# Kernel optimization log

Measured on AMD Instinct MI355X. Metric: run time of the kernel, lower is better.

The kernel has to match this reference:

```python
import jax, jax.numpy as jnp
import numpy as np

C = 256      # MSA_channels
PC = 256     # pair_channels
G = 4        # groups
GP = C // G  # group_planes
FF = 4 * C
EPS = 1e-5


def layernorm(x, w, b):
    mu = jnp.mean(x, axis=-1, keepdims=True)
    var = jnp.mean(jnp.square(x - mu), axis=-1, keepdims=True)
    return (x - mu) * jax.lax.rsqrt(var + EPS) * w + b


def setup_inputs() -> dict:
    key = jax.random.key(0)
    ks = jax.random.split(key, 12)
    N, D, L = 1, 64, 512
    s = lambda fan_in: 1.0 / np.sqrt(fan_in)
    return {
        "msa_matrix": jax.random.normal(ks[0], (N, D, L, C), jnp.float32),
        "rr_edge": jax.random.normal(ks[1], (N, L, L, PC), jnp.float32),
        "ln_msa_w": jnp.ones((C,), jnp.float32),
        "ln_msa_b": jnp.zeros((C,), jnp.float32),
        "ln_rr_w": jnp.ones((PC,), jnp.float32),
        "ln_rr_b": jnp.zeros((PC,), jnp.float32),
        "WA": jax.random.normal(ks[2], (PC, G), jnp.float32) * s(PC),
        "bA": jnp.zeros((G,), jnp.float32),
        "WV": jax.random.normal(ks[3], (C, C), jnp.float32) * s(C),
        "bV": jnp.zeros((C,), jnp.float32),
        "WO": jax.random.normal(ks[4], (C, C), jnp.float32) * s(C),
        "bO": jnp.zeros((C,), jnp.float32),
        "ln_ff_w": jnp.ones((C,), jnp.float32),
        "ln_ff_b": jnp.zeros((C,), jnp.float32),
        "W1": jax.random.normal(ks[5], (C, FF), jnp.float32) * s(C),
        "b1": jnp.zeros((FF,), jnp.float32),
        "W2": jax.random.normal(ks[6], (FF, C), jnp.float32) * s(FF),
        "b2": jnp.zeros((C,), jnp.float32),
    }


def reference(msa_matrix, rr_edge, ln_msa_w, ln_msa_b, ln_rr_w, ln_rr_b,
              WA, bA, WV, bV, WO, bO, ln_ff_w, ln_ff_b, W1, b1, W2, b2):
    N, D, L, _ = msa_matrix.shape
    raw = msa_matrix
    m = layernorm(msa_matrix, ln_msa_w, ln_msa_b)          # [N,D,L,C]
    E = 0.5 * (rr_edge + jnp.swapaxes(rr_edge, 1, 2))      # symmetrize [N,L,L,PC]
    E = layernorm(E, ln_rr_w, ln_rr_b)
    A = jax.nn.softmax(E @ WA + bA, axis=2)                # [N,L,L,G], softmax over key dim j
    V = (m @ WV + bV).reshape(N, D, L, G, GP)              # [N,D,L,G,GP]
    agg = jnp.einsum('nijg,ndjgc->ndigc', A, V).reshape(N, D, L, C)
    out = agg @ WO + bO
    x = raw + out                                          # residual (dropout = identity at eval)
    h = layernorm(x, ln_ff_w, ln_ff_b)                     # FFN with pre-LN + residual
    return x + (jax.nn.relu(h @ W1 + b1) @ W2 + b2)
```

## Files before the change

### kernel.cpp

```cpp
#include <hip/hip_runtime.h>
#include <hip/hip_bf16.h>

typedef __bf16 bf16;
typedef bf16 bf16x8 __attribute__((ext_vector_type(8)));
typedef bf16 bf16x4v __attribute__((ext_vector_type(4)));
typedef float f32x4 __attribute__((ext_vector_type(4)));

#define LN_EPS 1e-5f

__device__ __forceinline__ void gload_lds16(const bf16* gsrc, bf16* ldst) {
  __builtin_amdgcn_global_load_lds(
      (const __attribute__((address_space(1))) void*)gsrc,
      (__attribute__((address_space(3))) void*)ldst, 16, 0, 0);
}

__global__ __launch_bounds__(256) void ln_rows_kernel(
    const float* __restrict__ in, const float* __restrict__ w,
    const float* __restrict__ b, bf16* __restrict__ out)
{
  int row = blockIdx.x * 4 + (threadIdx.x >> 6);
  int lane = threadIdx.x & 63;
  const float4* p = (const float4*)(in + (size_t)row * 256);
  float4 v = p[lane];
  float s = v.x + v.y + v.z + v.w;
  float q = v.x*v.x + v.y*v.y + v.z*v.z + v.w*v.w;
  #pragma unroll
  for (int o = 32; o; o >>= 1) { s += __shfl_xor(s, o); q += __shfl_xor(q, o); }
  float mu = s * (1.0f/256.0f);
  float rs = rsqrtf(q*(1.0f/256.0f) - mu*mu + LN_EPS);
  float4 wv = ((const float4*)w)[lane];
  float4 bv = ((const float4*)b)[lane];
  bf16x4v o4;
  o4[0] = (bf16)((v.x - mu)*rs*wv.x + bv.x);
  o4[1] = (bf16)((v.y - mu)*rs*wv.y + bv.y);
  o4[2] = (bf16)((v.z - mu)*rs*wv.z + bv.z);
  o4[3] = (bf16)((v.w - mu)*rs*wv.w + bv.w);
  *(bf16x4v*)(out + (size_t)row * 256 + lane * 4) = o4;
}

__global__ __launch_bounds__(256) void transpose_all_kernel(
    const float* __restrict__ WV, const float* __restrict__ WO,
    const float* __restrict__ W1, const float* __restrict__ W2,
    bf16* __restrict__ WVt, bf16* __restrict__ WOt,
    bf16* __restrict__ W1t, bf16* __restrict__ W2t)
{
  __shared__ float tile[32][33];
  int id = blockIdx.x;
  const float* in; bf16* out; int R, C, tpr;
  if (id < 64)       { in = WV; out = WVt; R = 256;  C = 256;  tpr = 8;  }
  else if (id < 128) { in = WO; out = WOt; R = 256;  C = 256;  tpr = 8;  id -= 64; }
  else if (id < 384) { in = W1; out = W1t; R = 256;  C = 1024; tpr = 32; id -= 128; }
  else               { in = W2; out = W2t; R = 1024; C = 256;  tpr = 8;  id -= 384; }
  int bc = (id % tpr) * 32, br = (id / tpr) * 32;
  int tx = threadIdx.x, ty = threadIdx.y;
  #pragma unroll
  for (int i = ty; i < 32; i += 8)
    tile[i][tx] = in[(size_t)(br + i) * C + bc + tx];
  __syncthreads();
  #pragma unroll
  for (int i = ty; i < 32; i += 8)
    out[(size_t)(bc + i) * R + br + tx] = (bf16)tile[tx][i];
}

__global__ __launch_bounds__(256) void sym_ln_wa_kernel(
    const float* __restrict__ rr, const float* __restrict__ w,
    const float* __restrict__ b, const float* __restrict__ WA,
    float* __restrict__ S)
{
  int rem = blockIdx.x; int ti = 0; int len = 32;
  while (rem >= len) { rem -= len; ti++; len--; }
  int tj = ti + rem;
  int wid = threadIdx.x >> 6, lane = threadIdx.x & 63;
  int c0 = lane * 4;
  float4 wv = ((const float4*)w)[lane];
  float4 bv = ((const float4*)b)[lane];
  const float4* wa4 = (const float4*)WA;
  float4 wa0 = wa4[c0+0], wa1 = wa4[c0+1], wa2 = wa4[c0+2], wa3 = wa4[c0+3];
  int pend = blockIdx.y * 64 + 64;
  for (int p = blockIdx.y * 64 + wid; p < pend; p += 4) {
    int i = ti*16 + (p >> 4), j = tj*16 + (p & 15);
    float4 a = ((const float4*)(rr + ((size_t)i*512 + j)*256))[lane];
    float4 c = ((const float4*)(rr + ((size_t)j*512 + i)*256))[lane];
    float ex = 0.5f*(a.x + c.x), ey = 0.5f*(a.y + c.y),
          ez = 0.5f*(a.z + c.z), ew = 0.5f*(a.w + c.w);
    float s = ex+ey+ez+ew;
    float q = ex*ex+ey*ey+ez*ez+ew*ew;
    #pragma unroll
    for (int o = 32; o; o >>= 1) { s += __shfl_xor(s, o); q += __shfl_xor(q, o); }
    float mu = s*(1.f/256.f);
    float rs = rsqrtf(q*(1.f/256.f) - mu*mu + LN_EPS);
    float nx = (ex-mu)*rs*wv.x + bv.x;
    float ny = (ey-mu)*rs*wv.y + bv.y;
    float nz = (ez-mu)*rs*wv.z + bv.z;
    float nw = (ew-mu)*rs*wv.w + bv.w;
    float g0 = nx*wa0.x + ny*wa1.x + nz*wa2.x + nw*wa3.x;
    float g1 = nx*wa0.y + ny*wa1.y + nz*wa2.y + nw*wa3.y;
    float g2 = nx*wa0.z + ny*wa1.z + nz*wa2.z + nw*wa3.z;
    float g3 = nx*wa0.w + ny*wa1.w + nz*wa2.w + nw*wa3.w;
    #pragma unroll
    for (int o = 32; o; o >>= 1) {
      g0 += __shfl_xor(g0, o); g1 += __shfl_xor(g1, o);
      g2 += __shfl_xor(g2, o); g3 += __shfl_xor(g3, o);
    }
    if (lane == 0) {
      float4 r4 = make_float4(g0, g1, g2, g3);
      ((float4*)S)[(size_t)i*512 + j] = r4;
      ((float4*)S)[(size_t)j*512 + i] = r4;
    }
  }
}

__global__ __launch_bounds__(256) void softmax_kernel(
    const float* __restrict__ S, bf16* __restrict__ Aout)
{
  int i = blockIdx.x * 4 + (threadIdx.x >> 6);
  int lane = threadIdx.x & 63;
  const float4* Sr = (const float4*)S + (size_t)i * 512;
  float4 s[8];
  float m0 = -1e30f, m1 = -1e30f, m2 = -1e30f, m3 = -1e30f;
  #pragma unroll
  for (int it = 0; it < 8; it++) {
    s[it] = Sr[lane + it*64];
    m0 = fmaxf(m0, s[it].x); m1 = fmaxf(m1, s[it].y);
    m2 = fmaxf(m2, s[it].z); m3 = fmaxf(m3, s[it].w);
  }
  #pragma unroll
  for (int o = 32; o; o >>= 1) {
    m0 = fmaxf(m0, __shfl_xor(m0, o)); m1 = fmaxf(m1, __shfl_xor(m1, o));
    m2 = fmaxf(m2, __shfl_xor(m2, o)); m3 = fmaxf(m3, __shfl_xor(m3, o));
  }
  float t0=0.f, t1=0.f, t2=0.f, t3=0.f;
  #pragma unroll
  for (int it = 0; it < 8; it++) {
    s[it].x = __expf(s[it].x - m0); t0 += s[it].x;
    s[it].y = __expf(s[it].y - m1); t1 += s[it].y;
    s[it].z = __expf(s[it].z - m2); t2 += s[it].z;
    s[it].w = __expf(s[it].w - m3); t3 += s[it].w;
  }
  #pragma unroll
  for (int o = 32; o; o >>= 1) {
    t0 += __shfl_xor(t0, o); t1 += __shfl_xor(t1, o);
    t2 += __shfl_xor(t2, o); t3 += __shfl_xor(t3, o);
  }
  t0 = 1.f/t0; t1 = 1.f/t1; t2 = 1.f/t2; t3 = 1.f/t3;
  bf16* A0 = Aout + (size_t)i * 512;
  #pragma unroll
  for (int it = 0; it < 8; it++) {
    int j = lane + it*64;
    A0[j]          = (bf16)(s[it].x * t0);
    A0[262144 + j] = (bf16)(s[it].y * t1);
    A0[524288 + j] = (bf16)(s[it].z * t2);
    A0[786432 + j] = (bf16)(s[it].w * t3);
  }
}

template<int MODE>
__global__ __launch_bounds__(256) void gemm_bt_kernel(
    const bf16* __restrict__ Aglob, const bf16* __restrict__ Bglob,
    void* __restrict__ outP, const float* __restrict__ bias,
    const float* __restrict__ resid, int M, int N, int K)
{
  __shared__ bf16 As[128 * 32];
  __shared__ bf16 Bs[128 * 32];
  int g = blockIdx.z;
  const bf16* Ag = Aglob;
  const bf16* Bg = Bglob;
  if (MODE == 1) { Ag += (size_t)g * 512 * 512; Bg += (size_t)g * 4096 * 512; }
  int bm = blockIdx.y * 128, bn = blockIdx.x * 128;
  int tid = threadIdx.x;
  int wid = tid >> 6, lane = tid & 63;
  int wm = (wid >> 1) * 64, wn = (wid & 1) * 64;
  f32x4 acc[4][4];
  #pragma unroll
  for (int mi = 0; mi < 4; mi++)
    #pragma unroll
    for (int ni = 0; ni < 4; ni++)
      acc[mi][ni] = (f32x4){0.f, 0.f, 0.f, 0.f};
  int c0 = wid * 2, c1 = wid * 2 + 1;
  int srow = lane >> 2;
  int scol = (lane & 3) * 8;
  const bf16* a0 = &Ag[(size_t)(bm + c0*16 + srow) * K + scol];
  const bf16* a1 = &Ag[(size_t)(bm + c1*16 + srow) * K + scol];
  const bf16* b0 = &Bg[(size_t)(bn + c0*16 + srow) * K + scol];
  const bf16* b1 = &Bg[(size_t)(bn + c1*16 + srow) * K + scol];
  int fr = lane & 15, fk = (lane >> 4) * 8;
  for (int k0 = 0; k0 < K; k0 += 32) {
    __syncthreads();
    gload_lds16(a0 + k0, &As[c0 * 512]);
    gload_lds16(a1 + k0, &As[c1 * 512]);
    gload_lds16(b0 + k0, &Bs[c0 * 512]);
    gload_lds16(b1 + k0, &Bs[c1 * 512]);
    __syncthreads();
    bf16x8 af[4], bf_[4];
    #pragma unroll
    for (int mi = 0; mi < 4; mi++) af[mi] = *(const bf16x8*)&As[(wm + mi*16 + fr) * 32 + fk];
    #pragma unroll
    for (int ni = 0; ni < 4; ni++) bf_[ni] = *(const bf16x8*)&Bs[(wn + ni*16 + fr) * 32 + fk];
    #pragma unroll
    for (int mi = 0; mi < 4; mi++)
      #pragma unroll
      for (int ni = 0; ni < 4; ni++)
        acc[mi][ni] = __builtin_amdgcn_mfma_f32_16x16x32_bf16(af[mi], bf_[ni], acc[mi][ni], 0, 0, 0);
  }
  int cn0 = lane & 15;
  int rq = (lane >> 4) * 4;
  #pragma unroll
  for (int mi = 0; mi < 4; mi++) {
    #pragma unroll
    for (int ni = 0; ni < 4; ni++) {
      int mb = bm + wm + mi*16 + rq;
      int nc = bn + wn + ni*16 + cn0;
      #pragma unroll
      for (int r = 0; r < 4; r++) {
        int mr = mb + r;
        float v = acc[mi][ni][r];
        if (MODE == 0) {
          v += bias[mr];
          int gg = mr >> 6, rp = mr & 63, d = nc >> 9, j = nc & 511;
          ((bf16*)outP)[((size_t)gg*4096 + d*64 + rp)*512 + j] = (bf16)v;
        } else if (MODE == 1) {
          int d = nc >> 6, c6 = nc & 63;
          ((bf16*)outP)[((size_t)d*512 + mr)*256 + g*64 + c6] = (bf16)v;
        } else {
          v += bias[nc] + resid[(size_t)mr * N + nc];
          ((float*)outP)[(size_t)mr * N + nc] = v;
        }
      }
    }
  }
}

__global__ __launch_bounds__(512, 2) void ffn_fused_kernel(
    const float* __restrict__ x, const float* __restrict__ lnw,
    const float* __restrict__ lnb, const bf16* __restrict__ W1t,
    const float* __restrict__ b1, const bf16* __restrict__ W2t,
    const float* __restrict__ b2, float* __restrict__ out)
{
  __shared__ __align__(16) char hbuf[128 * 512];
  __shared__ __align__(16) char tbuf[128 * 512];
  __shared__ __align__(16) bf16 Bs[256 * 32];
  int tid = threadIdx.x;
  int wid = tid >> 6, lane = tid & 63;
  size_t row0 = (size_t)blockIdx.x * 128;

  {
    float4 wv = ((const float4*)lnw)[lane];
    float4 bv = ((const float4*)lnb)[lane];
    for (int it = 0; it < 16; it++) {
      int row = wid * 16 + it;
      float4 v = ((const float4*)(x + (row0 + row) * 256))[lane];
      float s = v.x+v.y+v.z+v.w, q = v.x*v.x+v.y*v.y+v.z*v.z+v.w*v.w;
      #pragma unroll
      for (int o = 32; o; o >>= 1) { s += __shfl_xor(s, o); q += __shfl_xor(q, o); }
      float mu = s * (1.f/256.f);
      float rs = rsqrtf(q*(1.f/256.f) - mu*mu + LN_EPS);
      bf16x4v o4;
      o4[0] = (bf16)((v.x-mu)*rs*wv.x + bv.x);
      o4[1] = (bf16)((v.y-mu)*rs*wv.y + bv.y);
      o4[2] = (bf16)((v.z-mu)*rs*wv.z + bv.z);
      o4[3] = (bf16)((v.w-mu)*rs*wv.w + bv.w);
      *(bf16x4v*)(hbuf + row*512 + ((lane*8) ^ ((row & 7) << 4))) = o4;
    }
  }
  __syncthreads();

  int wm = (wid >> 2) * 64;
  int wn = (wid & 3) * 64;
  int fr = lane & 15;
  int fk2 = ((lane >> 4) * 8) * 2;
  int cn0 = lane & 15, rq = (lane >> 4) * 4;
  int arow[4], asw[4], boff[4];
  #pragma unroll
  for (int mi = 0; mi < 4; mi++) {
    arow[mi] = wm + mi*16 + fr;
    asw[mi]  = (arow[mi] & 7) << 4;
  }
  #pragma unroll
  for (int ni = 0; ni < 4; ni++) {
    int br = wn + ni*16 + fr;
    boff[ni] = br*64 + (fk2 ^ (((br >> 1) & 3) << 4));
  }
  int srow = tid >> 2;
  int ps = tid & 3;

  f32x4 acc2[4][4];
  #pragma unroll
  for (int mi = 0; mi < 4; mi++)
    #pragma unroll
    for (int ni = 0; ni < 4; ni++)
      acc2[mi][ni] = (f32x4){0.f, 0.f, 0.f, 0.f};

  for (int cf = 0; cf < 4; cf++) {
    f32x4 acc1[4][4];
    #pragma unroll
    for (int mi = 0; mi < 4; mi++)
      #pragma unroll
      for (int ni = 0; ni < 4; ni++)
        acc1[mi][ni] = (f32x4){0.f, 0.f, 0.f, 0.f};
    for (int k0 = 0; k0 < 256; k0 += 32) {
      __syncthreads();
      #pragma unroll
      for (int q = 0; q < 2; q++) {
        int r = q*128 + srow;
        int ls = ps ^ ((r >> 1) & 3);
        gload_lds16(W1t + (size_t)(cf*256 + r) * 256 + k0 + ls*8,
                    Bs + q*4096 + wid*512);
      }
      __syncthreads();
      bf16x8 af[4], bf_[4];
      #pragma unroll
      for (int mi = 0; mi < 4; mi++)
        af[mi] = *(const bf16x8*)(hbuf + arow[mi]*512 + ((k0*2 + fk2) ^ asw[mi]));
      #pragma unroll
      for (int ni = 0; ni < 4; ni++)
        bf_[ni] = *(const bf16x8*)((const char*)Bs + boff[ni]);
      #pragma unroll
      for (int mi = 0; mi < 4; mi++)
        #pragma unroll
        for (int ni = 0; ni < 4; ni++)
          acc1[mi][ni] = __builtin_amdgcn_mfma_f32_16x16x32_bf16(af[mi], bf_[ni], acc1[mi][ni], 0, 0, 0);
    }
    __syncthreads();
    #pragma unroll
    for (int ni = 0; ni < 4; ni++) {
      int col = wn + ni*16 + cn0;
      float bb = b1[cf*256 + col];
      #pragma unroll
      for (int mi = 0; mi < 4; mi++) {
        #pragma unroll
        for (int r = 0; r < 4; r++) {
          int row = wm + mi*16 + rq + r;
          float v = fmaxf(acc1[mi][ni][r] + bb, 0.f);
          *(bf16*)(tbuf + row*512 + ((col*2) ^ ((row & 7) << 4))) = (bf16)v;
        }
      }
    }
    for (int k0 = 0; k0 < 256; k0 += 32) {
      __syncthreads();
      #pragma unroll
      for (int q = 0; q < 2; q++) {
        int r = q*128 + srow;
        int ls = ps ^ ((r >> 1) & 3);
        gload_lds16(W2t + (size_t)r * 1024 + cf*256 + k0 + ls*8,
                    Bs + q*4096 + wid*512);
      }
      __syncthreads();
      bf16x8 af[4], bf_[4];
      #pragma unroll
      for (int mi = 0; mi < 4; mi++)
        af[mi] = *(const bf16x8*)(tbuf + arow[mi]*512 + ((k0*2 + fk2) ^ asw[mi]));
      #pragma unroll
      for (int ni = 0; ni < 4; ni++)
        bf_[ni] = *(const bf16x8*)((const char*)Bs + boff[ni]);
      #pragma unroll
      for (int mi = 0; mi < 4; mi++)
        #pragma unroll
        for (int ni = 0; ni < 4; ni++)
          acc2[mi][ni] = __builtin_amdgcn_mfma_f32_16x16x32_bf16(af[mi], bf_[ni], acc2[mi][ni], 0, 0, 0);
    }
  }
  #pragma unroll
  for (int ni = 0; ni < 4; ni++) {
    int col = wn + ni*16 + cn0;
    float bb = b2[col];
    #pragma unroll
    for (int mi = 0; mi < 4; mi++) {
      #pragma unroll
      for (int r = 0; r < 4; r++) {
        size_t grow = row0 + wm + mi*16 + rq + r;
        out[grow*256 + col] = x[grow*256 + col] + acc2[mi][ni][r] + bb;
      }
    }
  }
}

extern "C" void kernel_launch(void* const* d_in, const int* in_sizes, int n_in,
                              void* d_out, int out_size, void* d_ws, size_t ws_size,
                              hipStream_t stream)
{
  (void)in_sizes; (void)n_in; (void)out_size; (void)ws_size;
  const float* msa = (const float*)d_in[0];
  const float* rr  = (const float*)d_in[1];
  const float* lmw = (const float*)d_in[2];
  const float* lmb = (const float*)d_in[3];
  const float* lrw = (const float*)d_in[4];
  const float* lrb = (const float*)d_in[5];
  const float* WA  = (const float*)d_in[6];
  const float* WV  = (const float*)d_in[8];
  const float* bV  = (const float*)d_in[9];
  const float* WO  = (const float*)d_in[10];
  const float* bO  = (const float*)d_in[11];
  const float* lfw = (const float*)d_in[12];
  const float* lfb = (const float*)d_in[13];
  const float* W1  = (const float*)d_in[14];
  const float* b1  = (const float*)d_in[15];
  const float* W2  = (const float*)d_in[16];
  const float* b2  = (const float*)d_in[17];
  float* out = (float*)d_out;
  char* ws = (char*)d_ws;
  float* S   = (float*)(ws + 0);
  bf16* Abuf = (bf16*)(ws + 4194304);
  bf16* m    = (bf16*)(ws + 6291456);
  bf16* Vt   = (bf16*)(ws + 23068672);
  bf16* agg  = (bf16*)(ws + 39845888);
  bf16* WVt  = (bf16*)(ws + 83886080);
  bf16* WOt  = WVt + 65536;
  bf16* W1t  = WOt + 65536;
  bf16* W2t  = W1t + 262144;

  transpose_all_kernel<<<640, dim3(32, 8), 0, stream>>>(WV, WO, W1, W2, WVt, WOt, W1t, W2t);

  ln_rows_kernel<<<8192, 256, 0, stream>>>(msa, lmw, lmb, m);
  sym_ln_wa_kernel<<<dim3(528, 4), 256, 0, stream>>>(rr, lrw, lrb, WA, S);
  gemm_bt_kernel<0><<<dim3(256, 2, 1), 256, 0, stream>>>(WVt, m, Vt, bV, nullptr, 256, 32768, 256);
  softmax_kernel<<<128, 256, 0, stream>>>(S, Abuf);
  gemm_bt_kernel<1><<<dim3(32, 4, 4), 256, 0, stream>>>(Abuf, Vt, agg, nullptr, nullptr, 512, 4096, 512);
  gemm_bt_kernel<2><<<dim3(2, 256, 1), 256, 0, stream>>>(agg, WOt, out, bO, msa, 32768, 256, 256);
  ffn_fused_kernel<<<256, 512, 0, stream>>>(out, lfw, lfb, W1t, b1, W2t, b2, out);
}
```

Measured before the change: 242.9 us.

## Double-buffer GEMM LDS tiles and load FFN weights directly from global

The generic bt GEMM gets two LDS buffers, so the next K-tile's global-to-LDS copy is issued before computing on the current one, with explicit vmcnt waits and barriers replacing the pair of __syncthreads per iteration. The fused FFN kernel stops staging W1/W2 tiles in LDS and reads B fragments straight from global memory, relying on cache reuse, which removes two barriers per K step and frees LDS for occupancy. The tradeoff is more global/L2 traffic per wave for the FFN, since each wave reloads weight fragments instead of sharing them through LDS. A barrier is added before the second FFN GEMM so tbuf is complete before it is read.

```diff
diff --git a/kernel.cpp b/kernel.cpp
--- a/kernel.cpp
+++ b/kernel.cpp
@@ -160,8 +160,8 @@
     void* __restrict__ outP, const float* __restrict__ bias,
     const float* __restrict__ resid, int M, int N, int K)
 {
-  __shared__ bf16 As[128 * 32];
-  __shared__ bf16 Bs[128 * 32];
+  __shared__ bf16 As[2][128 * 32];
+  __shared__ bf16 Bs[2][128 * 32];
   int g = blockIdx.z;
   const bf16* Ag = Aglob;
   const bf16* Bg = Bglob;
@@ -184,23 +184,38 @@
   const bf16* b0 = &Bg[(size_t)(bn + c0*16 + srow) * K + scol];
   const bf16* b1 = &Bg[(size_t)(bn + c1*16 + srow) * K + scol];
   int fr = lane & 15, fk = (lane >> 4) * 8;
-  for (int k0 = 0; k0 < K; k0 += 32) {
-    __syncthreads();
-    gload_lds16(a0 + k0, &As[c0 * 512]);
-    gload_lds16(a1 + k0, &As[c1 * 512]);
-    gload_lds16(b0 + k0, &Bs[c0 * 512]);
-    gload_lds16(b1 + k0, &Bs[c1 * 512]);
-    __syncthreads();
+  int nt = K >> 5;
+  gload_lds16(a0, &As[0][c0 * 512]);
+  gload_lds16(a1, &As[0][c1 * 512]);
+  gload_lds16(b0, &Bs[0][c0 * 512]);
+  gload_lds16(b1, &Bs[0][c1 * 512]);
+  int cur = 0;
+  for (int t = 0; t < nt; t++) {
+    if (t + 1 < nt) {
+      int k1 = (t + 1) << 5;
+      gload_lds16(a0 + k1, &As[cur ^ 1][c0 * 512]);
+      gload_lds16(a1 + k1, &As[cur ^ 1][c1 * 512]);
+      gload_lds16(b0 + k1, &Bs[cur ^ 1][c0 * 512]);
+      gload_lds16(b1 + k1, &Bs[cur ^ 1][c1 * 512]);
+      asm volatile("s_waitcnt vmcnt(4)" ::: "memory");
+    } else {
+      asm volatile("s_waitcnt vmcnt(0)" ::: "memory");
+    }
+    __builtin_amdgcn_s_barrier();
+    __builtin_amdgcn_sched_barrier(0);
     bf16x8 af[4], bf_[4];
     #pragma unroll
-    for (int mi = 0; mi < 4; mi++) af[mi] = *(const bf16x8*)&As[(wm + mi*16 + fr) * 32 + fk];
-    #pragma unroll
-    for (int ni = 0; ni < 4; ni++) bf_[ni] = *(const bf16x8*)&Bs[(wn + ni*16 + fr) * 32 + fk];
+    for (int mi = 0; mi < 4; mi++) af[mi] = *(const bf16x8*)&As[cur][(wm + mi*16 + fr) * 32 + fk];
+    #pragma unroll
+    for (int ni = 0; ni < 4; ni++) bf_[ni] = *(const bf16x8*)&Bs[cur][(wn + ni*16 + fr) * 32 + fk];
     #pragma unroll
     for (int mi = 0; mi < 4; mi++)
       #pragma unroll
       for (int ni = 0; ni < 4; ni++)
         acc[mi][ni] = __builtin_amdgcn_mfma_f32_16x16x32_bf16(af[mi], bf_[ni], acc[mi][ni], 0, 0, 0);
+    __builtin_amdgcn_sched_barrier(0);
+    __builtin_amdgcn_s_barrier();
+    cur ^= 1;
   }
   int cn0 = lane & 15;
   int rq = (lane >> 4) * 4;
@@ -238,7 +253,6 @@
 {
   __shared__ __align__(16) char hbuf[128 * 512];
   __shared__ __align__(16) char tbuf[128 * 512];
-  __shared__ __align__(16) bf16 Bs[256 * 32];
   int tid = threadIdx.x;
   int wid = tid >> 6, lane = tid & 63;
   size_t row0 = (size_t)blockIdx.x * 128;
@@ -267,21 +281,17 @@
   int wm = (wid >> 2) * 64;
   int wn = (wid & 3) * 64;
   int fr = lane & 15;
-  int fk2 = ((lane >> 4) * 8) * 2;
+  int fk = (lane >> 4) * 8;
+  int fk2 = fk * 2;
   int cn0 = lane & 15, rq = (lane >> 4) * 4;
-  int arow[4], asw[4], boff[4];
+  int arow[4], asw[4], brow[4];
   #pragma unroll
   for (int mi = 0; mi < 4; mi++) {
     arow[mi] = wm + mi*16 + fr;
     asw[mi]  = (arow[mi] & 7) << 4;
   }
   #pragma unroll
-  for (int ni = 0; ni < 4; ni++) {
-    int br = wn + ni*16 + fr;
-    boff[ni] = br*64 + (fk2 ^ (((br >> 1) & 3) << 4));
-  }
-  int srow = tid >> 2;
-  int ps = tid & 3;
+  for (int ni = 0; ni < 4; ni++) brow[ni] = wn + ni*16 + fr;
 
   f32x4 acc2[4][4];
   #pragma unroll
@@ -297,23 +307,15 @@
       #pragma unroll
       for (int ni = 0; ni < 4; ni++)
         acc1[mi][ni] = (f32x4){0.f, 0.f, 0.f, 0.f};
+    #pragma unroll 2
     for (int k0 = 0; k0 < 256; k0 += 32) {
-      __syncthreads();
-      #pragma unroll
-      for (int q = 0; q < 2; q++) {
-        int r = q*128 + srow;
-        int ls = ps ^ ((r >> 1) & 3);
-        gload_lds16(W1t + (size_t)(cf*256 + r) * 256 + k0 + ls*8,
-                    Bs + q*4096 + wid*512);
-      }
-      __syncthreads();
       bf16x8 af[4], bf_[4];
+      #pragma unroll
+      for (int ni = 0; ni < 4; ni++)
+        bf_[ni] = *(const bf16x8*)&W1t[(size_t)(cf*256 + brow[ni]) * 256 + k0 + fk];
       #pragma unroll
       for (int mi = 0; mi < 4; mi++)
         af[mi] = *(const bf16x8*)(hbuf + arow[mi]*512 + ((k0*2 + fk2) ^ asw[mi]));
-      #pragma unroll
-      for (int ni = 0; ni < 4; ni++)
-        bf_[ni] = *(const bf16x8*)((const char*)Bs + boff[ni]);
       #pragma unroll
       for (int mi = 0; mi < 4; mi++)
         #pragma unroll
@@ -335,23 +337,16 @@
         }
       }
     }
+    __syncthreads();
+    #pragma unroll 2
     for (int k0 = 0; k0 < 256; k0 += 32) {
-      __syncthreads();
-      #pragma unroll
-      for (int q = 0; q < 2; q++) {
-        int r = q*128 + srow;
-        int ls = ps ^ ((r >> 1) & 3);
-        gload_lds16(W2t + (size_t)r * 1024 + cf*256 + k0 + ls*8,
-                    Bs + q*4096 + wid*512);
-      }
-      __syncthreads();
       bf16x8 af[4], bf_[4];
+      #pragma unroll
+      for (int ni = 0; ni < 4; ni++)
+        bf_[ni] = *(const bf16x8*)&W2t[(size_t)brow[ni] * 1024 + cf*256 + k0 + fk];
       #pragma unroll
       for (int mi = 0; mi < 4; mi++)
         af[mi] = *(const bf16x8*)(tbuf + arow[mi]*512 + ((k0*2 + fk2) ^ asw[mi]));
-      #pragma unroll
-      for (int ni = 0; ni < 4; ni++)
-        bf_[ni] = *(const bf16x8*)((const char*)Bs + boff[ni]);
       #pragma unroll
       for (int mi = 0; mi < 4; mi++)
         #pragma unroll
```

New measurement: 242.1 us. No clear change (-0.3%).
